# Kernel tuning notes

Hardware: AMD Instinct MI355X
Metric: run time of the kernel (lower is better)

## Reference

```python
import jax, jax.numpy as jnp
import numpy as np

N = 100000
E = 1000000
IN_C = 256
HID = 64
OUT = 64
NEG_SLOPE = 0.2


def setup_inputs() -> dict:
    key = jax.random.key(0)
    ks = jax.random.split(key, 12)
    x = jax.random.normal(ks[0], (N, IN_C), dtype=jnp.float32)
    edge_index = jax.random.randint(ks[1], (2, E), 0, N, dtype=jnp.int64)
    s = 1.0 / np.sqrt(IN_C)
    W1 = jax.random.uniform(ks[2], (IN_C, HID), jnp.float32, -s, s)
    a1_src = jax.random.uniform(ks[3], (HID,), jnp.float32, -s, s)
    a1_dst = jax.random.uniform(ks[4], (HID,), jnp.float32, -s, s)
    b1 = jnp.zeros((HID,), jnp.float32)
    s2 = 1.0 / np.sqrt(HID)
    W2 = jax.random.uniform(ks[5], (HID, OUT), jnp.float32, -s2, s2)
    a2_src = jax.random.uniform(ks[6], (OUT,), jnp.float32, -s2, s2)
    a2_dst = jax.random.uniform(ks[7], (OUT,), jnp.float32, -s2, s2)
    b2 = jnp.zeros((OUT,), jnp.float32)
    return {"x": x, "edge_index": edge_index, "W1": W1, "a1_src": a1_src,
            "a1_dst": a1_dst, "b1": b1, "W2": W2, "a2_src": a2_src,
            "a2_dst": a2_dst, "b2": b2}


def gat_conv(x, W, a_src, a_dst, b, src, dst):
    h = x @ W                              # [N, d]
    alpha_s = h @ a_src                    # [N]
    alpha_d = h @ a_dst                    # [N]
    e = jax.nn.leaky_relu(alpha_s[src] + alpha_d[dst], NEG_SLOPE)  # [E]
    # segment softmax over incoming edges of each destination node
    e_max = jax.lax.stop_gradient(jax.ops.segment_max(e, dst, num_segments=N))
    ex = jnp.exp(e - e_max[dst])
    denom = jax.ops.segment_sum(ex, dst, num_segments=N)
    alpha = ex / (denom[dst] + 1e-16)      # [E]
    out = jax.ops.segment_sum(alpha[:, None] * h[src], dst, num_segments=N)
    return out + b


def reference(x, edge_index, W1, a1_src, a1_dst, b1, W2, a2_src, a2_dst, b2):
    src, dst = edge_index[0], edge_index[1]
    # dropout(p=0.6) is identity in eval mode
    h = jax.nn.relu(gat_conv(x, W1, a1_src, a1_dst, b1, src, dst))
    out = gat_conv(h, W2, a2_src, a2_dst, b2, src, dst)
    return out
```

## Files before the change

kernel.cpp:

```cpp
#include <hip/hip_runtime.h>
#include <math.h>

#define HID 64
#define BSH 9
#define NPB 512
#define EPB 4096

typedef __attribute__((ext_vector_type(8))) short bf16x8;
typedef __attribute__((ext_vector_type(4))) float f32x4;
typedef __attribute__((ext_vector_type(4))) unsigned int u32x4;

__device__ __forceinline__ unsigned short f2bf(float f) {
    unsigned u = __float_as_uint(f);
    unsigned r = u + 0x7FFF + ((u >> 16) & 1);
    return (unsigned short)(r >> 16);
}
__device__ __forceinline__ float bf2f(unsigned short b) {
    return __uint_as_float(((unsigned)b) << 16);
}


__global__ __launch_bounds__(256) void count_wt_kernel(const int* __restrict__ edst,
                                                       int* __restrict__ bcnt, int E_, int NB,
                                                       int gbk,
                                                       const float* __restrict__ W1,
                                                       unsigned short* __restrict__ Wt1, int K1,
                                                       const float* __restrict__ W2,
                                                       unsigned short* __restrict__ Wt2, int K2) {
    __shared__ int hist[256];
    int t = threadIdx.x;
    int b = blockIdx.x;
    if (b < gbk) {
        hist[t] = 0;
        __syncthreads();
        int base = b * EPB;
#pragma unroll
        for (int r = 0; r < EPB / 256; ++r) {
            int i = base + r * 256 + t;
            if (i < E_) atomicAdd(&hist[edst[i] >> BSH], 1);
        }
        __syncthreads();
        if (t < NB && hist[t]) atomicAdd(&bcnt[t], hist[t]);
    } else if (b < gbk + 64) {
        int k = (b - gbk) * 4 + (t >> 6);
        int n = t & 63;
        if (k < K1) Wt1[(size_t)n * K1 + k] = f2bf(W1[(size_t)k * 64 + n]);
    } else {
        int k = (b - gbk - 64) * 4 + (t >> 6);
        int n = t & 63;
        if (k < K2) Wt2[(size_t)n * K2 + k] = f2bf(W2[(size_t)k * 64 + n]);
    }
}

__global__ __launch_bounds__(256) void scan_nb(const int* __restrict__ bcnt,
                                               int* __restrict__ bbase,
                                               int* __restrict__ bcur, int NB) {
    __shared__ int sd[256];
    int t = threadIdx.x;
    int v = (t < NB) ? bcnt[t] : 0;
    sd[t] = v;
    __syncthreads();
    for (int o = 1; o < 256; o <<= 1) {
        int u = (t >= o) ? sd[t - o] : 0;
        __syncthreads();
        sd[t] += u;
        __syncthreads();
    }
    int ex = sd[t] - v;
    if (t < NB) {
        bbase[t] = ex;
        bcur[t] = ex;
    }
    if (t == 0) bbase[NB] = sd[NB - 1];
}

__device__ void scatter_body(char* smem, int b, const int* __restrict__ esrc,
                             const int* __restrict__ edst, int* __restrict__ bcur,
                             int2* __restrict__ ebuf, int E_, int NB) {
    int* hist = (int*)smem;
    int* chunk = hist + 256;
    int* lcur = chunk + 256;
    int t = threadIdx.x;
    hist[t] = 0;
    lcur[t] = 0;
    __syncthreads();
    int base = b * EPB;
    int s[EPB / 256], d[EPB / 256];
#pragma unroll
    for (int r = 0; r < EPB / 256; ++r) {
        int i = base + r * 256 + t;
        if (i < E_) {
            s[r] = esrc[i];
            d[r] = edst[i];
            atomicAdd(&hist[d[r] >> BSH], 1);
        } else {
            d[r] = -1;
        }
    }
    __syncthreads();
    if (t < NB) chunk[t] = hist[t] ? atomicAdd(&bcur[t], hist[t]) : 0;
    __syncthreads();
#pragma unroll
    for (int r = 0; r < EPB / 256; ++r) {
        if (d[r] >= 0) {
            int bk = d[r] >> BSH;
            int pos = chunk[bk] + atomicAdd(&lcur[bk], 1);
            ebuf[pos] = make_int2(s[r], d[r]);
        }
    }
}

__global__ __launch_bounds__(256) void csr_build(const int2* __restrict__ ebuf,
                                                 const int* __restrict__ bbase,
                                                 int* __restrict__ off,
                                                 int* __restrict__ srcs, int Nv, int NB) {
    __shared__ int dhist[NPB], dbase[NPB], psum[256];
    int b = blockIdx.x, t = threadIdx.x;
    int e0 = bbase[b], e1 = bbase[b + 1];
#pragma unroll
    for (int j = t; j < NPB; j += 256) dhist[j] = 0;
    __syncthreads();
    for (int i = e0 + t; i < e1; i += 256) {
        int d = ebuf[i].y;
        atomicAdd(&dhist[d & (NPB - 1)], 1);
    }
    __syncthreads();
    int a0 = dhist[2 * t], a1 = dhist[2 * t + 1];
    psum[t] = a0 + a1;
    __syncthreads();
    for (int o = 1; o < 256; o <<= 1) {
        int u = (t >= o) ? psum[t - o] : 0;
        __syncthreads();
        psum[t] += u;
        __syncthreads();
    }
    int ex = psum[t] - (a0 + a1);
    dbase[2 * t] = ex;
    dbase[2 * t + 1] = ex + a0;
    __syncthreads();
    for (int j = t; j < NPB; j += 256) {
        int node = (b << BSH) + j;
        if (node < Nv) off[node] = e0 + dbase[j];
    }
    if (b == NB - 1 && t == 0) off[Nv] = e1;
    __syncthreads();
    for (int i = e0 + t; i < e1; i += 256) {
        int2 p = ebuf[i];
        int pos = atomicAdd(&dbase[p.y & (NPB - 1)], 1);
        srcs[e0 + pos] = p.x;
    }
}


template <int K, bool BF16IN>
__device__ void gemm_body(char* smem, int bid, const void* __restrict__ Xv,
                          const unsigned short* __restrict__ Wt,
                          const float* __restrict__ a_s, const float* __restrict__ a_d,
                          unsigned short* __restrict__ C, float* __restrict__ as_,
                          float* __restrict__ ad_, int Nrows) {
    constexpr int KPAD = K + 8;
    constexpr int XPAD = 72;
    unsigned short* Ws = (unsigned short*)smem;
    unsigned short* Xs = (unsigned short*)(smem + (size_t)64 * KPAD * 2);

    const float* Xf = (const float*)Xv;
    const unsigned short* Xb = (const unsigned short*)Xv;

    int t = threadIdx.x;
    int n0 = bid * 128;
    int lane = t & 63;
    int w = t >> 6;
    int m = lane & 15;
    int q = lane >> 4;
    int base = n0 + w * 32;

    constexpr int KC8 = K / 8;
    for (int i = t; i < 64 * KC8; i += 256) {
        int n = i / KC8;
        int kc = i % KC8;
        u32x4 v = *(const u32x4*)(Wt + (size_t)n * K + kc * 8);
        *(u32x4*)(&Ws[n * KPAD + kc * 8]) = v;
    }

    f32x4 acc[2][4];
#pragma unroll
    for (int mi = 0; mi < 2; ++mi)
#pragma unroll
        for (int ct = 0; ct < 4; ++ct) acc[mi][ct] = (f32x4){0.f, 0.f, 0.f, 0.f};

    for (int k0 = 0; k0 < K; k0 += 64) {
        if (!BF16IN) {
#pragma unroll
            for (int i = 0; i < 8; ++i) {
                int idx = i * 256 + t;
                int row = idx >> 4;
                int kq = (idx & 15) * 4;
                int gn = n0 + row;
                if (gn >= Nrows) gn = Nrows - 1;
                float4 v = *(const float4*)(Xf + (size_t)gn * K + k0 + kq);
                ushort4 bb;
                bb.x = f2bf(v.x); bb.y = f2bf(v.y); bb.z = f2bf(v.z); bb.w = f2bf(v.w);
                *(ushort4*)(&Xs[row * XPAD + kq]) = bb;
            }
        } else {
#pragma unroll
            for (int i = 0; i < 4; ++i) {
                int idx = i * 256 + t;
                int row = idx >> 3;
                int kq = (idx & 7) * 8;
                int gn = n0 + row;
                if (gn >= Nrows) gn = Nrows - 1;
                u32x4 v = *(const u32x4*)(Xb + (size_t)gn * K + k0 + kq);
                *(u32x4*)(&Xs[row * XPAD + kq]) = v;
            }
        }
        __syncthreads();
#pragma unroll
        for (int ks = 0; ks < 64; ks += 32) {
            bf16x8 a0 = *(const bf16x8*)(&Xs[(w * 32 + m) * XPAD + ks + q * 8]);
            bf16x8 a1 = *(const bf16x8*)(&Xs[(w * 32 + 16 + m) * XPAD + ks + q * 8]);
#pragma unroll
            for (int ct = 0; ct < 4; ++ct) {
                bf16x8 bv = *(const bf16x8*)(&Ws[(ct * 16 + m) * KPAD + k0 + ks + q * 8]);
                acc[0][ct] = __builtin_amdgcn_mfma_f32_16x16x32_bf16(a0, bv, acc[0][ct], 0, 0, 0);
                acc[1][ct] = __builtin_amdgcn_mfma_f32_16x16x32_bf16(a1, bv, acc[1][ct], 0, 0, 0);
            }
        }
        __syncthreads();
    }

    float sa0 = a_s[m], sa1 = a_s[16 + m], sa2 = a_s[32 + m], sa3 = a_s[48 + m];
    float da0 = a_d[m], da1 = a_d[16 + m], da2 = a_d[32 + m], da3 = a_d[48 + m];

#pragma unroll
    for (int mi = 0; mi < 2; ++mi) {
#pragma unroll
        for (int r = 0; r < 4; ++r) {
            int row = base + mi * 16 + q * 4 + r;
            if (row < Nrows) {
                size_t ro = (size_t)row * 64 + m;
                C[ro]      = f2bf(acc[mi][0][r]);
                C[ro + 16] = f2bf(acc[mi][1][r]);
                C[ro + 32] = f2bf(acc[mi][2][r]);
                C[ro + 48] = f2bf(acc[mi][3][r]);
            }
        }
        float vs[4], vd[4];
#pragma unroll
        for (int r = 0; r < 4; ++r) {
            float s = acc[mi][0][r] * sa0 + acc[mi][1][r] * sa1 +
                      acc[mi][2][r] * sa2 + acc[mi][3][r] * sa3;
            float d = acc[mi][0][r] * da0 + acc[mi][1][r] * da1 +
                      acc[mi][2][r] * da2 + acc[mi][3][r] * da3;
#pragma unroll
            for (int o = 1; o < 16; o <<= 1) {
                s += __shfl_xor(s, o);
                d += __shfl_xor(d, o);
            }
            vs[r] = s;
            vd[r] = d;
        }
        if (m < 4) {
            int row = base + mi * 16 + q * 4 + m;
            float wvs = (m == 0) ? vs[0] : (m == 1) ? vs[1] : (m == 2) ? vs[2] : vs[3];
            float wvd = (m == 0) ? vd[0] : (m == 1) ? vd[1] : (m == 2) ? vd[2] : vd[3];
            if (row < Nrows) {
                as_[row] = wvs;
                ad_[row] = wvd;
            }
        }
    }
}

__global__ __launch_bounds__(256) void gemm1_scatter(const float* __restrict__ X,
                                                     const unsigned short* __restrict__ Wt,
                                                     const float* __restrict__ a_s,
                                                     const float* __restrict__ a_d,
                                                     unsigned short* __restrict__ C,
                                                     float* __restrict__ as_,
                                                     float* __restrict__ ad_, int Nrows,
                                                     const int* __restrict__ esrc,
                                                     const int* __restrict__ edst,
                                                     int* __restrict__ bcur,
                                                     int2* __restrict__ ebuf, int E_, int NB,
                                                     int gblocks) {
    extern __shared__ char smem[];
    if ((int)blockIdx.x < gblocks) {
        gemm_body<256, false>(smem, blockIdx.x, X, Wt, a_s, a_d, C, as_, ad_, Nrows);
    } else {
        scatter_body(smem, blockIdx.x - gblocks, esrc, edst, bcur, ebuf, E_, NB);
    }
}

__global__ __launch_bounds__(256) void gemm2_kernel(const unsigned short* __restrict__ X,
                                                    const unsigned short* __restrict__ Wt,
                                                    const float* __restrict__ a_s,
                                                    const float* __restrict__ a_d,
                                                    unsigned short* __restrict__ C,
                                                    float* __restrict__ as_,
                                                    float* __restrict__ ad_, int Nrows) {
    extern __shared__ char smem[];
    gemm_body<64, true>(smem, blockIdx.x, X, Wt, a_s, a_d, C, as_, ad_, Nrows);
}


template <bool RELU_BF16OUT>
__global__ __launch_bounds__(256) void agg_kernel(const unsigned short* __restrict__ H,
                                                  const float* __restrict__ as_,
                                                  const float* __restrict__ ad_,
                                                  const float* __restrict__ bias,
                                                  const int* __restrict__ off,
                                                  const int* __restrict__ srcs,
                                                  void* __restrict__ outp, int Nrows) {
    int d = blockIdx.x * 4 + (threadIdx.x >> 6);
    int lane = threadIdx.x & 63;
    if (d >= Nrows) return;
    int begin = off[d], end = off[d + 1];
    float adv = ad_[d];
    int g = lane >> 4;
    int c4 = (lane & 15) * 4;
    float4 acc = {0.f, 0.f, 0.f, 0.f};
    float lsum = 0.f;

    for (int bbase = begin; bbase < end; bbase += 64) {
        int cnt = end - bbase;
        if (cnt > 64) cnt = 64;
        int s = 0;
        float p = 0.f;
        if (lane < cnt) {
            s = srcs[bbase + lane];
            float xv = as_[s] + adv;
            xv = (xv > 0.f) ? xv : 0.2f * xv;
            p = __expf(xv);
        }
        lsum += p;
        int nb = (cnt + 3) & ~3;
        for (int j = 0; j < nb; j += 4) {
            int sv = __shfl(s, j + g);
            float pv = __shfl(p, j + g);
            ushort4 hv = *(const ushort4*)(H + (size_t)sv * HID + c4);
            acc.x += pv * bf2f(hv.x);
            acc.y += pv * bf2f(hv.y);
            acc.z += pv * bf2f(hv.z);
            acc.w += pv * bf2f(hv.w);
        }
    }
#pragma unroll
    for (int o = 16; o <= 32; o <<= 1) {
        acc.x += __shfl_xor(acc.x, o);
        acc.y += __shfl_xor(acc.y, o);
        acc.z += __shfl_xor(acc.z, o);
        acc.w += __shfl_xor(acc.w, o);
    }
#pragma unroll
    for (int o = 32; o; o >>= 1) lsum += __shfl_xor(lsum, o);
    if (g == 0) {
        float inv = 1.f / (lsum + 1e-16f);
        float4 b4 = *(const float4*)(bias + c4);
        float o0 = acc.x * inv + b4.x;
        float o1 = acc.y * inv + b4.y;
        float o2 = acc.z * inv + b4.z;
        float o3 = acc.w * inv + b4.w;
        if (RELU_BF16OUT) {
            ushort4 ov;
            ov.x = f2bf(fmaxf(o0, 0.f));
            ov.y = f2bf(fmaxf(o1, 0.f));
            ov.z = f2bf(fmaxf(o2, 0.f));
            ov.w = f2bf(fmaxf(o3, 0.f));
            *(ushort4*)((unsigned short*)outp + (size_t)d * HID + c4) = ov;
        } else {
            *(float4*)((float*)outp + (size_t)d * HID + c4) = make_float4(o0, o1, o2, o3);
        }
    }
}


extern "C" void kernel_launch(void* const* d_in, const int* in_sizes, int n_in,
                              void* d_out, int out_size, void* d_ws, size_t ws_size,
                              hipStream_t stream) {
    const float* x      = (const float*)d_in[0];
    const int*   edge   = (const int*)d_in[1];
    const float* W1     = (const float*)d_in[2];
    const float* a1_src = (const float*)d_in[3];
    const float* a1_dst = (const float*)d_in[4];
    const float* b1     = (const float*)d_in[5];
    const float* W2     = (const float*)d_in[6];
    const float* a2_src = (const float*)d_in[7];
    const float* a2_dst = (const float*)d_in[8];
    const float* b2     = (const float*)d_in[9];
    float* out = (float*)d_out;

    const int N = in_sizes[0] / 256;
    const int E = in_sizes[1] / 2;
    const int IN_C = 256;
    const int NB = (N + NPB - 1) >> BSH;

    char* w = (char*)d_ws;
    auto alloc = [&](size_t bytes) {
        char* p = w;
        w += (bytes + 255) & ~(size_t)255;
        return p;
    };
    int*            off   = (int*)alloc((size_t)(N + 1) * 4);
    int*            srcs  = (int*)alloc((size_t)E * 4);
    int2*           ebuf  = (int2*)alloc((size_t)E * 8);
    int*            bcnt  = (int*)alloc(256 * 4);
    int*            bbase = (int*)alloc(257 * 4);
    int*            bcur  = (int*)alloc(256 * 4);
    unsigned short* h1    = (unsigned short*)alloc((size_t)N * HID * 2);
    unsigned short* hB    = (unsigned short*)alloc((size_t)N * HID * 2);
    float*          as_   = (float*)alloc((size_t)N * 4);
    float*          ad_   = (float*)alloc((size_t)N * 4);
    unsigned short* Wt1   = (unsigned short*)alloc((size_t)IN_C * 64 * 2);
    unsigned short* Wt2   = (unsigned short*)alloc((size_t)64 * 64 * 2);

    const int* esrc = edge;
    const int* edst = edge + E;

    hipMemsetAsync(bcnt, 0, 256 * 4, stream);

    int gbk = (E + EPB - 1) / EPB;
    int gblocks = (N + 127) / 128;
    int ablocks = (N + 3) / 4;

    count_wt_kernel<<<gbk + 64 + 16, 256, 0, stream>>>(edst, bcnt, E, NB, gbk,
                                                       W1, Wt1, IN_C, W2, Wt2, 64);
    scan_nb<<<1, 256, 0, stream>>>(bcnt, bbase, bcur, NB);

    size_t smem1 = (size_t)64 * (256 + 8) * 2 + (size_t)128 * 72 * 2;
    gemm1_scatter<<<gblocks + gbk, 256, smem1, stream>>>(x, Wt1, a1_src, a1_dst, h1, as_, ad_, N,
                                                         esrc, edst, bcur, ebuf, E, NB, gblocks);
    csr_build<<<NB, 256, 0, stream>>>(ebuf, bbase, off, srcs, N, NB);
    agg_kernel<true><<<ablocks, 256, 0, stream>>>(h1, as_, ad_, b1, off, srcs, hB, N);
    size_t smem2 = (size_t)64 * (64 + 8) * 2 + (size_t)128 * 72 * 2;
    gemm2_kernel<<<gblocks, 256, smem2, stream>>>(hB, Wt2, a2_src, a2_dst, h1, as_, ad_, N);
    agg_kernel<false><<<ablocks, 256, 0, stream>>>(h1, as_, ad_, b2, off, srcs, out, N);
}
```

Baseline: 332.3 us.

## Split fused gemm/scatter kernel and read weights from global instead of LDS

The fused gemm1+scatter launch is split back into a separate scatter kernel and a templated GEMM kernel launched after CSR build. The GEMM no longer stages W into LDS; the B operand is read straight from global memory (L1/L2 cached), which cuts LDS use to the X tile and lets launch_bounds(256,4) target higher occupancy. In exchange it loses the overlap between GEMM and scatter blocks within one launch and adds repeated global loads of W per k-step.

```diff
diff --git a/kernel.cpp b/kernel.cpp
--- a/kernel.cpp
+++ b/kernel.cpp
@@ -74,17 +74,16 @@
     if (t == 0) bbase[NB] = sd[NB - 1];
 }
 
-__device__ void scatter_body(char* smem, int b, const int* __restrict__ esrc,
-                             const int* __restrict__ edst, int* __restrict__ bcur,
-                             int2* __restrict__ ebuf, int E_, int NB) {
-    int* hist = (int*)smem;
-    int* chunk = hist + 256;
-    int* lcur = chunk + 256;
+__global__ __launch_bounds__(256) void scatter_kernel(const int* __restrict__ esrc,
+                                                      const int* __restrict__ edst,
+                                                      int* __restrict__ bcur,
+                                                      int2* __restrict__ ebuf, int E_, int NB) {
+    __shared__ int hist[256], chunk[256], lcur[256];
     int t = threadIdx.x;
     hist[t] = 0;
     lcur[t] = 0;
     __syncthreads();
-    int base = b * EPB;
+    int base = blockIdx.x * EPB;
     int s[EPB / 256], d[EPB / 256];
 #pragma unroll
     for (int r = 0; r < EPB / 256; ++r) {
@@ -153,34 +152,26 @@
 
 
 template <int K, bool BF16IN>
-__device__ void gemm_body(char* smem, int bid, const void* __restrict__ Xv,
-                          const unsigned short* __restrict__ Wt,
-                          const float* __restrict__ a_s, const float* __restrict__ a_d,
-                          unsigned short* __restrict__ C, float* __restrict__ as_,
-                          float* __restrict__ ad_, int Nrows) {
-    constexpr int KPAD = K + 8;
+__global__ __launch_bounds__(256, 4) void gemm_kernel(const void* __restrict__ Xv,
+                                                      const unsigned short* __restrict__ Wt,
+                                                      const float* __restrict__ a_s,
+                                                      const float* __restrict__ a_d,
+                                                      unsigned short* __restrict__ C,
+                                                      float* __restrict__ as_,
+                                                      float* __restrict__ ad_, int Nrows) {
     constexpr int XPAD = 72;
-    unsigned short* Ws = (unsigned short*)smem;
-    unsigned short* Xs = (unsigned short*)(smem + (size_t)64 * KPAD * 2);
+    __shared__ __align__(16) unsigned short Xs[128 * XPAD];
 
     const float* Xf = (const float*)Xv;
     const unsigned short* Xb = (const unsigned short*)Xv;
 
     int t = threadIdx.x;
-    int n0 = bid * 128;
+    int n0 = blockIdx.x * 128;
     int lane = t & 63;
     int w = t >> 6;
     int m = lane & 15;
     int q = lane >> 4;
     int base = n0 + w * 32;
-
-    constexpr int KC8 = K / 8;
-    for (int i = t; i < 64 * KC8; i += 256) {
-        int n = i / KC8;
-        int kc = i % KC8;
-        u32x4 v = *(const u32x4*)(Wt + (size_t)n * K + kc * 8);
-        *(u32x4*)(&Ws[n * KPAD + kc * 8]) = v;
-    }
 
     f32x4 acc[2][4];
 #pragma unroll
@@ -221,7 +212,7 @@
             bf16x8 a1 = *(const bf16x8*)(&Xs[(w * 32 + 16 + m) * XPAD + ks + q * 8]);
 #pragma unroll
             for (int ct = 0; ct < 4; ++ct) {
-                bf16x8 bv = *(const bf16x8*)(&Ws[(ct * 16 + m) * KPAD + k0 + ks + q * 8]);
+                bf16x8 bv = *(const bf16x8*)(Wt + (size_t)(ct * 16 + m) * K + k0 + ks + q * 8);
                 acc[0][ct] = __builtin_amdgcn_mfma_f32_16x16x32_bf16(a0, bv, acc[0][ct], 0, 0, 0);
                 acc[1][ct] = __builtin_amdgcn_mfma_f32_16x16x32_bf16(a1, bv, acc[1][ct], 0, 0, 0);
             }
@@ -270,37 +261,6 @@
             }
         }
     }
-}
-
-__global__ __launch_bounds__(256) void gemm1_scatter(const float* __restrict__ X,
-                                                     const unsigned short* __restrict__ Wt,
-                                                     const float* __restrict__ a_s,
-                                                     const float* __restrict__ a_d,
-                                                     unsigned short* __restrict__ C,
-                                                     float* __restrict__ as_,
-                                                     float* __restrict__ ad_, int Nrows,
-                                                     const int* __restrict__ esrc,
-                                                     const int* __restrict__ edst,
-                                                     int* __restrict__ bcur,
-                                                     int2* __restrict__ ebuf, int E_, int NB,
-                                                     int gblocks) {
-    extern __shared__ char smem[];
-    if ((int)blockIdx.x < gblocks) {
-        gemm_body<256, false>(smem, blockIdx.x, X, Wt, a_s, a_d, C, as_, ad_, Nrows);
-    } else {
-        scatter_body(smem, blockIdx.x - gblocks, esrc, edst, bcur, ebuf, E_, NB);
-    }
-}
-
-__global__ __launch_bounds__(256) void gemm2_kernel(const unsigned short* __restrict__ X,
-                                                    const unsigned short* __restrict__ Wt,
-                                                    const float* __restrict__ a_s,
-                                                    const float* __restrict__ a_d,
-                                                    unsigned short* __restrict__ C,
-                                                    float* __restrict__ as_,
-                                                    float* __restrict__ ad_, int Nrows) {
-    extern __shared__ char smem[];
-    gemm_body<64, true>(smem, blockIdx.x, X, Wt, a_s, a_d, C, as_, ad_, Nrows);
 }
 
 
@@ -426,13 +386,12 @@
     count_wt_kernel<<<gbk + 64 + 16, 256, 0, stream>>>(edst, bcnt, E, NB, gbk,
                                                        W1, Wt1, IN_C, W2, Wt2, 64);
     scan_nb<<<1, 256, 0, stream>>>(bcnt, bbase, bcur, NB);
-
-    size_t smem1 = (size_t)64 * (256 + 8) * 2 + (size_t)128 * 72 * 2;
-    gemm1_scatter<<<gblocks + gbk, 256, smem1, stream>>>(x, Wt1, a1_src, a1_dst, h1, as_, ad_, N,
-                                                         esrc, edst, bcur, ebuf, E, NB, gblocks);
+    scatter_kernel<<<gbk, 256, 0, stream>>>(esrc, edst, bcur, ebuf, E, NB);
     csr_build<<<NB, 256, 0, stream>>>(ebuf, bbase, off, srcs, N, NB);
+
+    gemm_kernel<256, false><<<gblocks, 256, 0, stream>>>(x, Wt1, a1_src, a1_dst, h1, as_, ad_, N);
     agg_kernel<true><<<ablocks, 256, 0, stream>>>(h1, as_, ad_, b1, off, srcs, hB, N);
-    size_t smem2 = (size_t)64 * (64 + 8) * 2 + (size_t)128 * 72 * 2;
-    gemm2_kernel<<<gblocks, 256, smem2, stream>>>(hB, Wt2, a2_src, a2_dst, h1, as_, ad_, N);
+
+    gemm_kernel<64, true><<<gblocks, 256, 0, stream>>>(hB, Wt2, a2_src, a2_dst, h1, as_, ad_, N);
     agg_kernel<false><<<ablocks, 256, 0, stream>>>(h1, as_, ad_, b2, off, srcs, out, N);
 }
```

After: 336.6 us. About the same (+1.3%).
